# Kernel optimization log

Measured on AMD Instinct MI355X. Metric: run time of the kernel, lower is better.

Reference implementation:

```python
import jax, jax.numpy as jnp
import numpy as np

WINDOW = 128  # window_size from init_kwargs
D = 1024      # input_dim
S = 8192      # seq_len


def setup_inputs() -> dict:
    key = jax.random.key(0)
    k1, k2, k3, k4, k5 = jax.random.split(key, 5)
    bound = 1.0 / np.sqrt(D)
    x = jax.random.normal(k1, (1, S, D), dtype=jnp.float32)
    Wq = jax.random.uniform(k2, (D, D), minval=-bound, maxval=bound, dtype=jnp.float32)
    bq = jax.random.uniform(k3, (D,), minval=-bound, maxval=bound, dtype=jnp.float32)
    Wk = jax.random.uniform(k4, (D, D), minval=-bound, maxval=bound, dtype=jnp.float32)
    bk = jax.random.uniform(k5, (D,), minval=-bound, maxval=bound, dtype=jnp.float32)
    return {"x": x, "Wq": Wq, "bq": bq, "Wk": Wk, "bk": bk}


def reference(x, Wq, bq, Wk, bk):
    # x: [1, S, D]  (original code only works with batch==1)
    xs = x[0]                          # [S, D]
    q = xs @ Wq.T + bq                 # [S, D]
    k = xs @ Wk.T + bk                 # [S, D]
    scores = q @ k.T                   # [S, S] dense, matches original buffer
    t = jnp.arange(S)[:, None]
    s = jnp.arange(S)[None, :]
    # original writes scores only for s in [t-WINDOW, t+WINDOW); elsewhere stays 0
    inwin = (s >= t - WINDOW) & (s < t + WINDOW)
    scores = jnp.where(inwin, scores, 0.0)
    attn = jax.nn.softmax(scores, axis=1)  # softmax INCLUDES the zero entries, as in original
    out = attn @ xs                    # [S, D]
    return out
```

## Files before the change

kernel.cpp:

```cpp
#include <hip/hip_runtime.h>

#define S 8192
#define D 1024
#define WINDOW 128
#define TQ 16
#define UMAX 288
#define BK 32
#define PAD 68
#define BAND 320

typedef __attribute__((ext_vector_type(8))) short short8;
typedef __attribute__((ext_vector_type(4))) float floatx4;
typedef __attribute__((ext_vector_type(4))) unsigned short ushort4v;
typedef unsigned short u16t;

__device__ __forceinline__ float wave_sum(float v) {
  #pragma unroll
  for (int off = 32; off > 0; off >>= 1) v += __shfl_xor(v, off, 64);
  return v;
}
__device__ __forceinline__ float wave_max(float v) {
  #pragma unroll
  for (int off = 32; off > 0; off >>= 1) v = fmaxf(v, __shfl_xor(v, off, 64));
  return v;
}
__device__ __forceinline__ unsigned int f2bf_rn(float f) {
  unsigned int u = __float_as_uint(f);
  return (u + 0x7fffu + ((u >> 16) & 1u)) >> 16;
}

#define GLDS(gp, lp) __builtin_amdgcn_global_load_lds( \
    (const __attribute__((address_space(1))) void*)(gp), \
    (__attribute__((address_space(3))) void*)(lp), 16, 0, 0)


__global__ __launch_bounds__(256) void wuv_kernel(
    const float* __restrict__ Wq, const float* __restrict__ Wk,
    const float* __restrict__ bq, const float* __restrict__ bk,
    float* __restrict__ uu, float* __restrict__ vv, float* __restrict__ cbuf,
    u16t* __restrict__ wqth, u16t* __restrict__ wqtl,
    u16t* __restrict__ wkth, u16t* __restrict__ wktl,
    float* __restrict__ zreg)
{
  __shared__ float tile[64][65];
  __shared__ float cr[4];
  const int t = threadIdx.x;
  if (blockIdx.z == 2) {
    if (blockIdx.y == 0) {
      if (blockIdx.x < 8) {
        const int i  = (blockIdx.x & 3) * 256 + t;
        const int nh = blockIdx.x >> 2;
        float us = 0.f, vs = 0.f;
        for (int n = nh * 512; n < nh * 512 + 512; ++n) {
          us += Wq[(size_t)n * D + i] * bk[n];
          vs += Wk[(size_t)n * D + i] * bq[n];
        }
        uu[(size_t)nh * D + i] = us;
        vv[(size_t)nh * D + i] = vs;
      } else if (blockIdx.x == 8) {
        float cs = 0.f;
        for (int n = t; n < D; n += 256) cs += bq[n] * bk[n];
        cs = wave_sum(cs);
        if ((t & 63) == 0) cr[t >> 6] = cs;
        __syncthreads();
        if (t == 0) cbuf[0] = cr[0] + cr[1] + cr[2] + cr[3];
      }
    } else {
      int fb  = (blockIdx.y - 1) * 16 + blockIdx.x;
      int idx = fb * 256 + t;
      if (idx < D + 2 * S) zreg[idx] = 0.f;
    }
    return;
  }
  const float* W = blockIdx.z ? Wk : Wq;
  u16t* oh = blockIdx.z ? wkth : wqth;
  u16t* ol = blockIdx.z ? wktl : wqtl;
  const int n0 = blockIdx.x * 64;
  const int i0 = blockIdx.y * 64;
  #pragma unroll
  for (int p = 0; p < 4; ++p) {
    int r = (t >> 4) + p * 16;
    int c = (t & 15) * 4;
    float4 vf = *(const float4*)(W + (size_t)(n0 + r) * D + i0 + c);
    tile[r][c+0] = vf.x; tile[r][c+1] = vf.y; tile[r][c+2] = vf.z; tile[r][c+3] = vf.w;
  }
  __syncthreads();
  #pragma unroll
  for (int p = 0; p < 4; ++p) {
    int ii = (t >> 4) + p * 16;
    int nn = (t & 15) * 4;
    ushort4v h, l;
    #pragma unroll
    for (int e = 0; e < 4; ++e) {
      float f = tile[nn + e][ii];
      unsigned int hb = f2bf_rn(f);
      float hf = __uint_as_float(hb << 16);
      h[e] = (u16t)hb;
      l[e] = (u16t)f2bf_rn(f - hf);
    }
    size_t idx = (size_t)(i0 + ii) * D + n0 + nn;
    *(ushort4v*)(oh + idx) = h;
    *(ushort4v*)(ol + idx) = l;
  }
}

__global__ __launch_bounds__(256) void prep_kernel(
    const float* __restrict__ x, const float* __restrict__ uu,
    const float* __restrict__ vv, u16t* __restrict__ xhi, u16t* __restrict__ xlo,
    u16t* __restrict__ xT, float* __restrict__ xsum,
    float* __restrict__ a, float* __restrict__ b)
{
  __shared__ float tile[64][65];
  const int s0 = blockIdx.x * 64;
  const int d0 = blockIdx.y * 64;
  const int t = threadIdx.x;
  #pragma unroll
  for (int p = 0; p < 4; ++p) {
    int r = (t >> 4) + p * 16;
    int c = (t & 15) * 4;
    float4 vf = *(const float4*)(x + (size_t)(s0 + r) * D + d0 + c);
    float f[4] = {vf.x, vf.y, vf.z, vf.w};
    tile[r][c+0] = vf.x; tile[r][c+1] = vf.y; tile[r][c+2] = vf.z; tile[r][c+3] = vf.w;
    ushort4v h, l;
    #pragma unroll
    for (int e = 0; e < 4; ++e) {
      unsigned int hb = f2bf_rn(f[e]);
      float hf = __uint_as_float(hb << 16);
      h[e] = (u16t)hb;
      l[e] = (u16t)f2bf_rn(f[e] - hf);
    }
    size_t idx = (size_t)(s0 + r) * D + d0 + c;
    *(ushort4v*)(xhi + idx) = h;
    *(ushort4v*)(xlo + idx) = l;
  }
  __syncthreads();
  #pragma unroll
  for (int p = 0; p < 4; ++p) {
    int dd = (t >> 4) + p * 16;
    int ss = (t & 15) * 4;
    ushort4v o;
    #pragma unroll
    for (int e = 0; e < 4; ++e) o[e] = (u16t)f2bf_rn(tile[ss + e][dd]);
    *(ushort4v*)(xT + (size_t)(d0 + dd) * S + s0 + ss) = o;
  }
  if (t < 64) {
    float s = 0.f;
    #pragma unroll 8
    for (int r = 0; r < 64; ++r) s += tile[r][t];
    atomicAdd(&xsum[d0 + t], s);
  } else if (t < 128) {
    int r = t - 64;
    float s = 0.f;
    for (int c = 0; c < 64; ++c) s += tile[r][c] * (uu[d0 + c] + uu[D + d0 + c]);
    atomicAdd(&a[s0 + r], s);
  } else if (t < 192) {
    int r = t - 128;
    float s = 0.f;
    for (int c = 0; c < 64; ++c) s += tile[r][c] * (vv[d0 + c] + vv[D + d0 + c]);
    atomicAdd(&b[s0 + r], s);
  }
}

__global__ __launch_bounds__(256) void m_kernel(
    const u16t* __restrict__ wqth, const u16t* __restrict__ wqtl,
    const u16t* __restrict__ wkth, const u16t* __restrict__ wktl,
    u16t* __restrict__ mh, u16t* __restrict__ ml)
{
  __shared__ __align__(16) u16t Mbuf[4][64 * BK];

  const int tid  = threadIdx.x;
  const int lane = tid & 63;
  const int wv   = tid >> 6;
  const int i0   = blockIdx.x * 64;
  const int j0   = blockIdx.y * 64;

  floatx4 acc[2][2] = {};
  const int m0w = (wv & 1) * 32;
  const int n0w = (wv >> 1) * 32;
  const int srow = lane >> 2;
  const int scolw = ((lane & 3) ^ ((lane >> 3) & 3)) * 8;
  const int rs    = (((lane >> 4) ^ ((lane >> 1) & 3)) * 8);

  for (int k0 = 0; k0 < D; k0 += BK) {
    __syncthreads();
    {
      const u16t* src = (wv == 0) ? wqth : (wv == 1) ? wqtl : (wv == 2) ? wkth : wktl;
      const int base  = (wv < 2) ? i0 : j0;
      #pragma unroll
      for (int sg = 0; sg < 4; ++sg) {
        int row = base + sg * 16 + srow;
        size_t g = (size_t)row * D + k0 + scolw;
        GLDS(src + g, &Mbuf[wv][sg * 512]);
      }
    }
    __syncthreads();
    short8 ah[2], al[2], bh[2], bl[2];
    #pragma unroll
    for (int t = 0; t < 2; ++t) {
      int ar = (m0w + t * 16 + (lane & 15)) * BK + rs;
      int br = (n0w + t * 16 + (lane & 15)) * BK + rs;
      ah[t] = *(const short8*)&Mbuf[0][ar];
      al[t] = *(const short8*)&Mbuf[1][ar];
      bh[t] = *(const short8*)&Mbuf[2][br];
      bl[t] = *(const short8*)&Mbuf[3][br];
    }
    #pragma unroll
    for (int mt = 0; mt < 2; ++mt)
      #pragma unroll
      for (int nt = 0; nt < 2; ++nt) {
        acc[mt][nt] = __builtin_amdgcn_mfma_f32_16x16x32_bf16(ah[mt], bh[nt], acc[mt][nt], 0, 0, 0);
        acc[mt][nt] = __builtin_amdgcn_mfma_f32_16x16x32_bf16(ah[mt], bl[nt], acc[mt][nt], 0, 0, 0);
        acc[mt][nt] = __builtin_amdgcn_mfma_f32_16x16x32_bf16(al[mt], bh[nt], acc[mt][nt], 0, 0, 0);
      }
  }
  #pragma unroll
  for (int mt = 0; mt < 2; ++mt)
    #pragma unroll
    for (int nt = 0; nt < 2; ++nt) {
      int j = j0 + n0w + nt * 16 + (lane & 15);
      int i = i0 + m0w + mt * 16 + (lane >> 4) * 4;
      #pragma unroll
      for (int r = 0; r < 4; ++r) {
        float f = acc[mt][nt][r];
        unsigned int hb = f2bf_rn(f);
        float hf = __uint_as_float(hb << 16);
        size_t idx = (size_t)(i + r) * D + j;
        mh[idx] = (u16t)hb;
        ml[idx] = (u16t)f2bf_rn(f - hf);
      }
    }
}

__global__ __launch_bounds__(256) void y_kernel(
    const u16t* __restrict__ xhi, const u16t* __restrict__ xlo,
    const u16t* __restrict__ mhp, const u16t* __restrict__ mlp,
    u16t* __restrict__ yh, u16t* __restrict__ yl)
{
  __shared__ __align__(16) u16t Ah[2 * 128 * BK];
  __shared__ __align__(16) u16t Al[2 * 128 * BK];
  __shared__ __align__(16) u16t Bh[2 * 128 * BK];
  __shared__ __align__(16) u16t Bl[2 * 128 * BK];

  const int tid  = threadIdx.x;
  const int lane = tid & 63;
  const int wv   = tid >> 6;
  const int s0   = blockIdx.x * 128;
  const int i0   = blockIdx.y * 128;

  floatx4 acc[4][4] = {};
  const int m0w  = (wv & 1) * 64;
  const int n0w  = (wv >> 1) * 64;
  const int srow = lane >> 2;
  const int scolw = ((lane & 3) ^ ((lane >> 3) & 3)) * 8;
  const int rs    = (((lane >> 4) ^ ((lane >> 1) & 3)) * 8);

  for (int k0 = 0; k0 < D; k0 += 64) {
    __syncthreads();
    #pragma unroll
    for (int h = 0; h < 2; ++h) {
      #pragma unroll
      for (int sg = 0; sg < 2; ++sg) {
        int seg  = wv * 2 + sg;
        int arow = s0 + seg * 16 + srow;
        int brow = i0 + seg * 16 + srow;
        size_t ga = (size_t)arow * D + k0 + h * 32 + scolw;
        size_t gb = (size_t)brow * D + k0 + h * 32 + scolw;
        int lb = h * 4096 + seg * 512;
        GLDS(xhi + ga, &Ah[lb]);
        GLDS(xlo + ga, &Al[lb]);
        GLDS(mhp + gb, &Bh[lb]);
        GLDS(mlp + gb, &Bl[lb]);
      }
    }
    __syncthreads();
    #pragma unroll
    for (int h = 0; h < 2; ++h) {
      short8 ah[4], al[4], bh[4], bl[4];
      #pragma unroll
      for (int t = 0; t < 4; ++t) {
        int ar = h * 4096 + (m0w + t * 16 + (lane & 15)) * BK + rs;
        int br = h * 4096 + (n0w + t * 16 + (lane & 15)) * BK + rs;
        ah[t] = *(const short8*)&Ah[ar];
        al[t] = *(const short8*)&Al[ar];
        bh[t] = *(const short8*)&Bh[br];
        bl[t] = *(const short8*)&Bl[br];
      }
      #pragma unroll
      for (int mt = 0; mt < 4; ++mt)
        #pragma unroll
        for (int nt = 0; nt < 4; ++nt) {
          acc[mt][nt] = __builtin_amdgcn_mfma_f32_16x16x32_bf16(ah[mt], bh[nt], acc[mt][nt], 0, 0, 0);
          acc[mt][nt] = __builtin_amdgcn_mfma_f32_16x16x32_bf16(ah[mt], bl[nt], acc[mt][nt], 0, 0, 0);
          acc[mt][nt] = __builtin_amdgcn_mfma_f32_16x16x32_bf16(al[mt], bh[nt], acc[mt][nt], 0, 0, 0);
        }
    }
  }
  #pragma unroll
  for (int mt = 0; mt < 4; ++mt)
    #pragma unroll
    for (int nt = 0; nt < 4; ++nt) {
      int i = i0 + n0w + nt * 16 + (lane & 15);
      int s = s0 + m0w + mt * 16 + (lane >> 4) * 4;
      #pragma unroll
      for (int r = 0; r < 4; ++r) {
        float f = acc[mt][nt][r];
        unsigned int hb = f2bf_rn(f);
        float hf = __uint_as_float(hb << 16);
        size_t idx = (size_t)(s + r) * D + i;
        yh[idx] = (u16t)hb;
        yl[idx] = (u16t)f2bf_rn(f - hf);
      }
    }
}

__global__ __launch_bounds__(256) void scores_kernel(
    const u16t* __restrict__ xhi, const u16t* __restrict__ xlo,
    const u16t* __restrict__ yh, const u16t* __restrict__ yl,
    const float* __restrict__ a, const float* __restrict__ b,
    const float* __restrict__ cbuf, float* __restrict__ band)
{
  __shared__ __align__(16) u16t Ah[2 * 64 * BK];
  __shared__ __align__(16) u16t Al[2 * 64 * BK];
  __shared__ __align__(16) u16t Bh[2 * 64 * BK];
  __shared__ __align__(16) u16t Bl[2 * 64 * BK];

  const int tid  = threadIdx.x;
  const int lane = tid & 63;
  const int wv   = tid >> 6;
  const int t0   = blockIdx.x * 64;
  const int jt   = blockIdx.y;
  const int s_base = t0 - 128 + jt * 64;
  const float cval = cbuf[0];

  floatx4 acc[2][2] = {};
  const int m0w  = (wv & 1) * 32;
  const int n0w  = (wv >> 1) * 32;
  const int srow = lane >> 2;
  const int scolw = ((lane & 3) ^ ((lane >> 3) & 3)) * 8;
  const int rs    = (((lane >> 4) ^ ((lane >> 1) & 3)) * 8);

  for (int k0 = 0; k0 < D; k0 += 64) {
    __syncthreads();
    #pragma unroll
    for (int h = 0; h < 2; ++h) {
      int arow = t0 + wv * 16 + srow;
      int brow = s_base + wv * 16 + srow;
      brow = min(max(brow, 0), S - 1);
      size_t ga = (size_t)arow * D + k0 + h * 32 + scolw;
      size_t gb = (size_t)brow * D + k0 + h * 32 + scolw;
      int lb = h * 2048 + wv * 512;
      GLDS(xhi + ga, &Ah[lb]);
      GLDS(xlo + ga, &Al[lb]);
      GLDS(yh + gb, &Bh[lb]);
      GLDS(yl + gb, &Bl[lb]);
    }
    __syncthreads();
    #pragma unroll
    for (int h = 0; h < 2; ++h) {
      short8 ah[2], al[2], bh[2], bl[2];
      #pragma unroll
      for (int t = 0; t < 2; ++t) {
        int ar = h * 2048 + (m0w + t * 16 + (lane & 15)) * BK + rs;
        int br = h * 2048 + (n0w + t * 16 + (lane & 15)) * BK + rs;
        ah[t] = *(const short8*)&Ah[ar];
        al[t] = *(const short8*)&Al[ar];
        bh[t] = *(const short8*)&Bh[br];
        bl[t] = *(const short8*)&Bl[br];
      }
      #pragma unroll
      for (int mt = 0; mt < 2; ++mt)
        #pragma unroll
        for (int nt = 0; nt < 2; ++nt) {
          acc[mt][nt] = __builtin_amdgcn_mfma_f32_16x16x32_bf16(ah[mt], bh[nt], acc[mt][nt], 0, 0, 0);
          acc[mt][nt] = __builtin_amdgcn_mfma_f32_16x16x32_bf16(ah[mt], bl[nt], acc[mt][nt], 0, 0, 0);
          acc[mt][nt] = __builtin_amdgcn_mfma_f32_16x16x32_bf16(al[mt], bh[nt], acc[mt][nt], 0, 0, 0);
        }
    }
  }
  #pragma unroll
  for (int mt = 0; mt < 2; ++mt)
    #pragma unroll
    for (int nt = 0; nt < 2; ++nt) {
      int n_loc = n0w + nt * 16 + (lane & 15);
      int s = s_base + n_loc;
      float bv = (s >= 0 && s < S) ? b[s] : 0.f;
      #pragma unroll
      for (int r = 0; r < 4; ++r) {
        int m_loc = m0w + mt * 16 + (lane >> 4) * 4 + r;
        int t = t0 + m_loc;
        bool inwin = (s >= t - WINDOW) && (s < t + WINDOW) && (s >= 0) && (s < S);
        float sv = inwin ? (acc[mt][nt][r] + a[t] + bv + cval) : 0.f;
        band[(size_t)t * BAND + jt * 64 + n_loc] = sv;
      }
    }
}

#define PSTR 328
__global__ __launch_bounds__(256) void pv_kernel(
    const float* __restrict__ band, const u16t* __restrict__ xT,
    const float* __restrict__ xsum, float* __restrict__ out)
{
  __shared__ __align__(16) u16t Pl[64 * PSTR];
  __shared__ __align__(16) u16t Bb[2 * 128 * BK];
  __shared__ float e0s[64];

  const int tid  = threadIdx.x;
  const int lane = tid & 63;
  const int wv   = tid >> 6;
  const int t0   = blockIdx.x * 64;
  const int d0   = blockIdx.y * 128;
  const int origin = t0 - 128;

  for (int it = 0; it < 16; ++it) {
    int rloc = it * 4 + wv;
    const float* row = band + (size_t)(t0 + rloc) * BAND;
    float v[5];
    float mx = 0.f;
    #pragma unroll
    for (int i = 0; i < 5; ++i) {
      v[i] = row[i * 64 + lane];
      mx = fmaxf(mx, v[i]);
    }
    mx = wave_max(mx);
    float e0 = __expf(-mx);
    float ss = 0.f;
    #pragma unroll
    for (int i = 0; i < 5; ++i) {
      v[i] = __expf(v[i] - mx);
      ss += v[i];
    }
    ss = wave_sum(ss);
    float dinv = 1.f / (ss + (float)(S - BAND) * e0);
    #pragma unroll
    for (int i = 0; i < 5; ++i)
      Pl[rloc * PSTR + i * 64 + lane] = (u16t)f2bf_rn((v[i] - e0) * dinv);
    if (lane == 0) e0s[rloc] = e0 * dinv;
  }

  floatx4 acc[2][4] = {};
  const int m0w  = (wv & 1) * 32;
  const int n0w  = (wv >> 1) * 64;
  const int srow = lane >> 2;
  const int scolw = ((lane & 3) ^ ((lane >> 3) & 3)) * 8;
  const int rs    = (((lane >> 4) ^ ((lane >> 1) & 3)) * 8);
  const int fr    = lane & 15;
  const int qA    = (lane >> 4) * 8;

  for (int k0 = 0; k0 < BAND; k0 += 64) {
    __syncthreads();
    #pragma unroll
    for (int h = 0; h < 2; ++h) {
      #pragma unroll
      for (int sg = 0; sg < 2; ++sg) {
        int seg  = wv * 2 + sg;
        int brow = d0 + seg * 16 + srow;
        int s_g  = origin + k0 + h * 32 + scolw;
        s_g = min(max(s_g, 0), S - 8);
        size_t gb = (size_t)brow * S + s_g;
        GLDS(xT + gb, &Bb[h * 4096 + seg * 512]);
      }
    }
    __syncthreads();
    #pragma unroll
    for (int h = 0; h < 2; ++h) {
      short8 af[2], bf[4];
      #pragma unroll
      for (int t = 0; t < 2; ++t)
        af[t] = *(const short8*)&Pl[(m0w + t * 16 + fr) * PSTR + k0 + h * 32 + qA];
      #pragma unroll
      for (int t = 0; t < 4; ++t)
        bf[t] = *(const short8*)&Bb[h * 4096 + (n0w + t * 16 + fr) * BK + rs];
      #pragma unroll
      for (int mt = 0; mt < 2; ++mt)
        #pragma unroll
        for (int nt = 0; nt < 4; ++nt)
          acc[mt][nt] = __builtin_amdgcn_mfma_f32_16x16x32_bf16(af[mt], bf[nt], acc[mt][nt], 0, 0, 0);
    }
  }
  #pragma unroll
  for (int mt = 0; mt < 2; ++mt)
    #pragma unroll
    for (int nt = 0; nt < 4; ++nt) {
      int n_g = d0 + n0w + nt * 16 + fr;
      float xs = xsum[n_g];
      #pragma unroll
      for (int r = 0; r < 4; ++r) {
        int rloc = m0w + mt * 16 + (lane >> 4) * 4 + r;
        out[(size_t)(t0 + rloc) * D + n_g] = acc[mt][nt][r] + e0s[rloc] * xs;
      }
    }
}

__global__ __launch_bounds__(256) void proj_kernel(
    const float* __restrict__ x, const float* __restrict__ Wq,
    const float* __restrict__ bqv, const float* __restrict__ Wk,
    const float* __restrict__ bkv, float* __restrict__ qout,
    float* __restrict__ kout)
{
  __shared__ __align__(16) float xs[BK][PAD];
  __shared__ __align__(16) float wqs[BK][PAD];
  __shared__ __align__(16) float wks[BK][PAD];
  const int tid = threadIdx.x;
  const int tx = tid & 15, ty = tid >> 4;
  const int t0 = blockIdx.x * 64, i0 = blockIdx.y * 64;
  float accq[4][4] = {}, acck[4][4] = {};
  const int lrow0 = tid >> 3, lc4 = (tid & 7) * 4;
  for (int k0 = 0; k0 < D; k0 += BK) {
    __syncthreads();
    #pragma unroll
    for (int p = 0; p < 2; ++p) {
      int row = lrow0 + p * 32;
      float4 a = *(const float4*)(x  + (size_t)(t0 + row) * D + k0 + lc4);
      float4 b = *(const float4*)(Wq + (size_t)(i0 + row) * D + k0 + lc4);
      float4 c = *(const float4*)(Wk + (size_t)(i0 + row) * D + k0 + lc4);
      xs [lc4+0][row]=a.x; xs [lc4+1][row]=a.y; xs [lc4+2][row]=a.z; xs [lc4+3][row]=a.w;
      wqs[lc4+0][row]=b.x; wqs[lc4+1][row]=b.y; wqs[lc4+2][row]=b.z; wqs[lc4+3][row]=b.w;
      wks[lc4+0][row]=c.x; wks[lc4+1][row]=c.y; wks[lc4+2][row]=c.z; wks[lc4+3][row]=c.w;
    }
    __syncthreads();
    #pragma unroll
    for (int kk = 0; kk < BK; ++kk) {
      float4 av = *(const float4*)&xs [kk][ty*4];
      float4 bv = *(const float4*)&wqs[kk][tx*4];
      float4 cv = *(const float4*)&wks[kk][tx*4];
      float a[4] = {av.x, av.y, av.z, av.w};
      float b[4] = {bv.x, bv.y, bv.z, bv.w};
      float c[4] = {cv.x, cv.y, cv.z, cv.w};
      #pragma unroll
      for (int r = 0; r < 4; ++r)
        #pragma unroll
        for (int cc = 0; cc < 4; ++cc) {
          accq[r][cc] = fmaf(a[r], b[cc], accq[r][cc]);
          acck[r][cc] = fmaf(a[r], c[cc], acck[r][cc]);
        }
    }
  }
  float4 bq4 = *(const float4*)(bqv + i0 + tx*4);
  float4 bk4 = *(const float4*)(bkv + i0 + tx*4);
  #pragma unroll
  for (int r = 0; r < 4; ++r) {
    int trow = t0 + ty*4 + r;
    float4 oq = { accq[r][0]+bq4.x, accq[r][1]+bq4.y, accq[r][2]+bq4.z, accq[r][3]+bq4.w };
    float4 ok = { acck[r][0]+bk4.x, acck[r][1]+bk4.y, acck[r][2]+bk4.z, acck[r][3]+bk4.w };
    *(float4*)(qout + (size_t)trow * D + i0 + tx*4) = oq;
    *(float4*)(kout + (size_t)trow * D + i0 + tx*4) = ok;
  }
}

__global__ __launch_bounds__(256) void colsum_kernel(const float* __restrict__ x,
                                                     float* __restrict__ xsum)
{
  int d = blockIdx.x * 256 + threadIdx.x;
  int tbase = blockIdx.y * 256;
  float s = 0.f;
  for (int t = 0; t < 256; ++t) s += x[(size_t)(tbase + t) * D + d];
  atomicAdd(&xsum[d], s);
}

__global__ __launch_bounds__(256) void attn_kernel(
    const float* __restrict__ x, const float* __restrict__ q,
    const float* __restrict__ kmat, const float* __restrict__ xsum,
    float* __restrict__ out)
{
  __shared__ __align__(16) float scl[TQ][UMAX];
  __shared__ float e0s[TQ], dinv[TQ];
  const int tid = threadIdx.x, lane = tid & 63, wv = tid >> 6;
  const int t0 = blockIdx.x * TQ;
  const int lo_u = max(0, t0 - WINDOW);
  const int hi_u = min(S, t0 + TQ - 1 + WINDOW);
  const int ucnt = hi_u - lo_u;
  for (int i = tid; i < TQ * UMAX; i += 256) (&scl[0][0])[i] = 0.f;
  __syncthreads();
  {
    const int tiB = wv * 4;
    float4 qf[4][4];
    #pragma unroll
    for (int g = 0; g < 4; ++g) {
      int t = t0 + tiB + g;
      #pragma unroll
      for (int j = 0; j < 4; ++j)
        qf[g][j] = *(const float4*)(q + (size_t)t * D + lane*4 + j*256);
    }
    const int wlo = max(0, t0 + tiB - WINDOW);
    const int whi = min(S, t0 + tiB + 3 + WINDOW);
    for (int s = wlo; s < whi; ++s) {
      float4 kf[4];
      #pragma unroll
      for (int j = 0; j < 4; ++j)
        kf[j] = *(const float4*)(kmat + (size_t)s * D + lane*4 + j*256);
      float acc[4];
      #pragma unroll
      for (int g = 0; g < 4; ++g) {
        float v = 0.f;
        #pragma unroll
        for (int j = 0; j < 4; ++j) {
          v = fmaf(qf[g][j].x, kf[j].x, v);
          v = fmaf(qf[g][j].y, kf[j].y, v);
          v = fmaf(qf[g][j].z, kf[j].z, v);
          v = fmaf(qf[g][j].w, kf[j].w, v);
        }
        acc[g] = v;
      }
      #pragma unroll
      for (int g = 0; g < 4; ++g) {
        float tot = wave_sum(acc[g]);
        int t = t0 + tiB + g;
        if (lane == 0 && s >= t - WINDOW && s < t + WINDOW)
          scl[tiB + g][s - lo_u] = tot;
      }
    }
  }
  __syncthreads();
  #pragma unroll
  for (int g = 0; g < 4; ++g) {
    int ti = wv * 4 + g;
    int t = t0 + ti;
    int lo = max(0, t - WINDOW), hi = min(S, t + WINDOW);
    int cnt = hi - lo, off = lo - lo_u;
    float m = 0.f;
    for (int i = lane; i < cnt; i += 64) m = fmaxf(m, scl[ti][off + i]);
    m = wave_max(m);
    float e0 = __expf(-m);
    float ssum = 0.f;
    for (int i = lane; i < cnt; i += 64) {
      float e = __expf(scl[ti][off + i] - m);
      ssum += e;
      scl[ti][off + i] = e - e0;
    }
    ssum = wave_sum(ssum);
    if (lane == 0) {
      dinv[ti] = 1.f / (ssum + (float)(S - cnt) * e0);
      e0s[ti] = e0;
    }
  }
  __syncthreads();
  {
    const int c4 = tid * 4;
    float4 acc[TQ];
    #pragma unroll
    for (int ti = 0; ti < TQ; ++ti) acc[ti] = make_float4(0.f, 0.f, 0.f, 0.f);
    for (int su = 0; su < ucnt; su += 4) {
      float4 xr[4];
      #pragma unroll
      for (int u = 0; u < 4; ++u)
        xr[u] = *(const float4*)(x + (size_t)(lo_u + su + u) * D + c4);
      #pragma unroll
      for (int ti = 0; ti < TQ; ++ti) {
        float4 w4 = *(const float4*)&scl[ti][su];
        float wvv[4] = {w4.x, w4.y, w4.z, w4.w};
        #pragma unroll
        for (int u = 0; u < 4; ++u) {
          acc[ti].x = fmaf(wvv[u], xr[u].x, acc[ti].x);
          acc[ti].y = fmaf(wvv[u], xr[u].y, acc[ti].y);
          acc[ti].z = fmaf(wvv[u], xr[u].z, acc[ti].z);
          acc[ti].w = fmaf(wvv[u], xr[u].w, acc[ti].w);
        }
      }
    }
    float4 xsv = *(const float4*)(xsum + c4);
    #pragma unroll
    for (int ti = 0; ti < TQ; ++ti) {
      float e0 = e0s[ti], di = dinv[ti];
      float4 o;
      o.x = (acc[ti].x + e0 * xsv.x) * di;
      o.y = (acc[ti].y + e0 * xsv.y) * di;
      o.z = (acc[ti].z + e0 * xsv.z) * di;
      o.w = (acc[ti].w + e0 * xsv.w) * di;
      *(float4*)(out + (size_t)(t0 + ti) * D + c4) = o;
    }
  }
}

extern "C" void kernel_launch(void* const* d_in, const int* in_sizes, int n_in,
                              void* d_out, int out_size, void* d_ws, size_t ws_size,
                              hipStream_t stream) {
  const float* x  = (const float*)d_in[0];
  const float* Wq = (const float*)d_in[1];
  const float* bq = (const float*)d_in[2];
  const float* Wk = (const float*)d_in[3];
  const float* bk = (const float*)d_in[4];
  float* outp = (float*)d_out;

  const size_t SD = (size_t)S * D;
  const size_t DD = (size_t)D * D;

  float* xsum = (float*)d_ws;
  float* a    = xsum + D;
  float* b    = a + S;
  float* uu   = b + S;
  float* vv   = uu + 2 * D;
  float* cbuf = vv + 2 * D;

  u16t* xhi  = (u16t*)(cbuf + 16);
  u16t* xlo  = xhi + SD;
  u16t* xT   = xlo + SD;
  u16t* wqth = xT + SD;
  u16t* wqtl = wqth + DD;
  u16t* wkth = wqtl + DD;
  u16t* wktl = wkth + DD;
  u16t* mh   = wktl + DD;
  u16t* ml   = mh + DD;
  u16t* yh   = ml + DD;
  u16t* yl   = yh + SD;
  float* band = (float*)(yl + SD);
  size_t needed = (size_t)((char*)(band + (size_t)S * BAND) - (char*)d_ws);

  if (ws_size >= needed) {
    wuv_kernel<<<dim3(16, 16, 3), 256, 0, stream>>>(
        Wq, Wk, bq, bk, uu, vv, cbuf, wqth, wqtl, wkth, wktl, xsum);
    prep_kernel<<<dim3(S / 64, D / 64), 256, 0, stream>>>(x, uu, vv, xhi, xlo, xT, xsum, a, b);
    m_kernel<<<dim3(D / 64, D / 64), 256, 0, stream>>>(wqth, wqtl, wkth, wktl, mh, ml);
    y_kernel<<<dim3(S / 128, D / 128), 256, 0, stream>>>(xhi, xlo, mh, ml, yh, yl);
    scores_kernel<<<dim3(S / 64, 5), 256, 0, stream>>>(xhi, xlo, yh, yl, a, b, cbuf, band);
    pv_kernel<<<dim3(S / 64, D / 128), 256, 0, stream>>>(band, xT, xsum, outp);
  } else {
    float* xs2  = (float*)d_ws;
    float* q    = xs2 + D;
    float* kbuf = q + SD;
    (void)hipMemsetAsync(xs2, 0, D * sizeof(float), stream);
    colsum_kernel<<<dim3(D / 256, S / 256), 256, 0, stream>>>(x, xs2);
    proj_kernel<<<dim3(S / 64, D / 64), 256, 0, stream>>>(x, Wq, bq, Wk, bk, q, kbuf);
    attn_kernel<<<S / TQ, 256, 0, stream>>>(x, q, kbuf, xs2, outp);
  }
}
```

Measured before the change: 293.2 us.

## Switch GEMMs to 32x32x16 MFMA and split softmax out of PV kernel

```diff
diff --git a/kernel.cpp b/kernel.cpp
--- a/kernel.cpp
+++ b/kernel.cpp
@@ -11,6 +11,7 @@
 
 typedef __attribute__((ext_vector_type(8))) short short8;
 typedef __attribute__((ext_vector_type(4))) float floatx4;
+typedef __attribute__((ext_vector_type(16))) float floatx16;
 typedef __attribute__((ext_vector_type(4))) unsigned short ushort4v;
 typedef unsigned short u16t;
 
@@ -174,12 +175,14 @@
   const int i0   = blockIdx.x * 64;
   const int j0   = blockIdx.y * 64;
 
-  floatx4 acc[2][2] = {};
+  floatx16 acc = {};
   const int m0w = (wv & 1) * 32;
   const int n0w = (wv >> 1) * 32;
   const int srow = lane >> 2;
   const int scolw = ((lane & 3) ^ ((lane >> 3) & 3)) * 8;
-  const int rs    = (((lane >> 4) ^ ((lane >> 1) & 3)) * 8);
+  const int rsw = (lane >> 1) & 3;
+  const int l31 = lane & 31;
+  const int khi = lane >> 5;
 
   for (int k0 = 0; k0 < D; k0 += BK) {
     __syncthreads();
@@ -194,41 +197,34 @@
       }
     }
     __syncthreads();
-    short8 ah[2], al[2], bh[2], bl[2];
-    #pragma unroll
-    for (int t = 0; t < 2; ++t) {
-      int ar = (m0w + t * 16 + (lane & 15)) * BK + rs;
-      int br = (n0w + t * 16 + (lane & 15)) * BK + rs;
-      ah[t] = *(const short8*)&Mbuf[0][ar];
-      al[t] = *(const short8*)&Mbuf[1][ar];
-      bh[t] = *(const short8*)&Mbuf[2][br];
-      bl[t] = *(const short8*)&Mbuf[3][br];
-    }
-    #pragma unroll
-    for (int mt = 0; mt < 2; ++mt)
-      #pragma unroll
-      for (int nt = 0; nt < 2; ++nt) {
-        acc[mt][nt] = __builtin_amdgcn_mfma_f32_16x16x32_bf16(ah[mt], bh[nt], acc[mt][nt], 0, 0, 0);
-        acc[mt][nt] = __builtin_amdgcn_mfma_f32_16x16x32_bf16(ah[mt], bl[nt], acc[mt][nt], 0, 0, 0);
-        acc[mt][nt] = __builtin_amdgcn_mfma_f32_16x16x32_bf16(al[mt], bh[nt], acc[mt][nt], 0, 0, 0);
-      }
-  }
-  #pragma unroll
-  for (int mt = 0; mt < 2; ++mt)
-    #pragma unroll
-    for (int nt = 0; nt < 2; ++nt) {
-      int j = j0 + n0w + nt * 16 + (lane & 15);
-      int i = i0 + m0w + mt * 16 + (lane >> 4) * 4;
-      #pragma unroll
-      for (int r = 0; r < 4; ++r) {
-        float f = acc[mt][nt][r];
-        unsigned int hb = f2bf_rn(f);
-        float hf = __uint_as_float(hb << 16);
-        size_t idx = (size_t)(i + r) * D + j;
-        mh[idx] = (u16t)hb;
-        ml[idx] = (u16t)f2bf_rn(f - hf);
-      }
-    }
+    #pragma unroll
+    for (int ks = 0; ks < 2; ++ks) {
+      int slot = ((ks * 2 + khi) ^ rsw) * 8;
+      int ar = (m0w + l31) * BK + slot;
+      int br = (n0w + l31) * BK + slot;
+      short8 ah = *(const short8*)&Mbuf[0][ar];
+      short8 al = *(const short8*)&Mbuf[1][ar];
+      short8 bh = *(const short8*)&Mbuf[2][br];
+      short8 bl = *(const short8*)&Mbuf[3][br];
+      acc = __builtin_amdgcn_mfma_f32_32x32x16_bf16(ah, bh, acc, 0, 0, 0);
+      acc = __builtin_amdgcn_mfma_f32_32x32x16_bf16(ah, bl, acc, 0, 0, 0);
+      acc = __builtin_amdgcn_mfma_f32_32x32x16_bf16(al, bh, acc, 0, 0, 0);
+    }
+  }
+  {
+    int j = j0 + n0w + l31;
+    int ib = i0 + m0w + 4 * khi;
+    #pragma unroll
+    for (int r = 0; r < 16; ++r) {
+      int i = ib + (r & 3) + 8 * (r >> 2);
+      float f = acc[r];
+      unsigned int hb = f2bf_rn(f);
+      float hf = __uint_as_float(hb << 16);
+      size_t idx = (size_t)i * D + j;
+      mh[idx] = (u16t)hb;
+      ml[idx] = (u16t)f2bf_rn(f - hf);
+    }
+  }
 }
 
 __global__ __launch_bounds__(256) void y_kernel(
@@ -247,12 +243,14 @@
   const int s0   = blockIdx.x * 128;
   const int i0   = blockIdx.y * 128;
 
-  floatx4 acc[4][4] = {};
+  floatx16 acc[2][2] = {};
   const int m0w  = (wv & 1) * 64;
   const int n0w  = (wv >> 1) * 64;
   const int srow = lane >> 2;
   const int scolw = ((lane & 3) ^ ((lane >> 3) & 3)) * 8;
-  const int rs    = (((lane >> 4) ^ ((lane >> 1) & 3)) * 8);
+  const int rsw = (lane >> 1) & 3;
+  const int l31 = lane & 31;
+  const int khi = lane >> 5;
 
   for (int k0 = 0; k0 < D; k0 += 64) {
     __syncthreads();
@@ -275,38 +273,43 @@
     __syncthreads();
     #pragma unroll
     for (int h = 0; h < 2; ++h) {
-      short8 ah[4], al[4], bh[4], bl[4];
-      #pragma unroll
-      for (int t = 0; t < 4; ++t) {
-        int ar = h * 4096 + (m0w + t * 16 + (lane & 15)) * BK + rs;
-        int br = h * 4096 + (n0w + t * 16 + (lane & 15)) * BK + rs;
-        ah[t] = *(const short8*)&Ah[ar];
-        al[t] = *(const short8*)&Al[ar];
-        bh[t] = *(const short8*)&Bh[br];
-        bl[t] = *(const short8*)&Bl[br];
-      }
-      #pragma unroll
-      for (int mt = 0; mt < 4; ++mt)
+      #pragma unroll
+      for (int ks = 0; ks < 2; ++ks) {
+        int slot = ((ks * 2 + khi) ^ rsw) * 8;
+        short8 ah[2], al[2], bh[2], bl[2];
         #pragma unroll
-        for (int nt = 0; nt < 4; ++nt) {
-          acc[mt][nt] = __builtin_amdgcn_mfma_f32_16x16x32_bf16(ah[mt], bh[nt], acc[mt][nt], 0, 0, 0);
-          acc[mt][nt] = __builtin_amdgcn_mfma_f32_16x16x32_bf16(ah[mt], bl[nt], acc[mt][nt], 0, 0, 0);
-          acc[mt][nt] = __builtin_amdgcn_mfma_f32_16x16x32_bf16(al[mt], bh[nt], acc[mt][nt], 0, 0, 0);
+        for (int t = 0; t < 2; ++t) {
+          int ar = h * 4096 + (m0w + t * 32 + l31) * BK + slot;
+          int br = h * 4096 + (n0w + t * 32 + l31) * BK + slot;
+          ah[t] = *(const short8*)&Ah[ar];
+          al[t] = *(const short8*)&Al[ar];
+          bh[t] = *(const short8*)&Bh[br];
+          bl[t] = *(const short8*)&Bl[br];
         }
-    }
-  }
-  #pragma unroll
-  for (int mt = 0; mt < 4; ++mt)
-    #pragma unroll
-    for (int nt = 0; nt < 4; ++nt) {
-      int i = i0 + n0w + nt * 16 + (lane & 15);
-      int s = s0 + m0w + mt * 16 + (lane >> 4) * 4;
-      #pragma unroll
-      for (int r = 0; r < 4; ++r) {
+        #pragma unroll
+        for (int mt = 0; mt < 2; ++mt)
+          #pragma unroll
+          for (int nt = 0; nt < 2; ++nt) {
+            acc[mt][nt] = __builtin_amdgcn_mfma_f32_32x32x16_bf16(ah[mt], bh[nt], acc[mt][nt], 0, 0, 0);
+            acc[mt][nt] = __builtin_amdgcn_mfma_f32_32x32x16_bf16(ah[mt], bl[nt], acc[mt][nt], 0, 0, 0);
+            acc[mt][nt] = __builtin_amdgcn_mfma_f32_32x32x16_bf16(al[mt], bh[nt], acc[mt][nt], 0, 0, 0);
+          }
+      }
+    }
+  }
+  #pragma unroll
+  for (int mt = 0; mt < 2; ++mt)
+    #pragma unroll
+    for (int nt = 0; nt < 2; ++nt) {
+      int i  = i0 + n0w + nt * 32 + l31;
+      int sb = s0 + m0w + mt * 32 + 4 * khi;
+      #pragma unroll
+      for (int r = 0; r < 16; ++r) {
+        int s = sb + (r & 3) + 8 * (r >> 2);
         float f = acc[mt][nt][r];
         unsigned int hb = f2bf_rn(f);
         float hf = __uint_as_float(hb << 16);
-        size_t idx = (size_t)(s + r) * D + i;
+        size_t idx = (size_t)s * D + i;
         yh[idx] = (u16t)hb;
         yl[idx] = (u16t)f2bf_rn(f - hf);
       }
@@ -332,12 +335,14 @@
   const int s_base = t0 - 128 + jt * 64;
   const float cval = cbuf[0];
 
-  floatx4 acc[2][2] = {};
+  floatx16 acc = {};
   const int m0w  = (wv & 1) * 32;
   const int n0w  = (wv >> 1) * 32;
   const int srow = lane >> 2;
   const int scolw = ((lane & 3) ^ ((lane >> 3) & 3)) * 8;
-  const int rs    = (((lane >> 4) ^ ((lane >> 1) & 3)) * 8);
+  const int rsw = (lane >> 1) & 3;
+  const int l31 = lane & 31;
+  const int khi = lane >> 5;
 
   for (int k0 = 0; k0 < D; k0 += 64) {
     __syncthreads();
@@ -357,52 +362,74 @@
     __syncthreads();
     #pragma unroll
     for (int h = 0; h < 2; ++h) {
-      short8 ah[2], al[2], bh[2], bl[2];
-      #pragma unroll
-      for (int t = 0; t < 2; ++t) {
-        int ar = h * 2048 + (m0w + t * 16 + (lane & 15)) * BK + rs;
-        int br = h * 2048 + (n0w + t * 16 + (lane & 15)) * BK + rs;
-        ah[t] = *(const short8*)&Ah[ar];
-        al[t] = *(const short8*)&Al[ar];
-        bh[t] = *(const short8*)&Bh[br];
-        bl[t] = *(const short8*)&Bl[br];
-      }
-      #pragma unroll
-      for (int mt = 0; mt < 2; ++mt)
-        #pragma unroll
-        for (int nt = 0; nt < 2; ++nt) {
-          acc[mt][nt] = __builtin_amdgcn_mfma_f32_16x16x32_bf16(ah[mt], bh[nt], acc[mt][nt], 0, 0, 0);
-          acc[mt][nt] = __builtin_amdgcn_mfma_f32_16x16x32_bf16(ah[mt], bl[nt], acc[mt][nt], 0, 0, 0);
-          acc[mt][nt] = __builtin_amdgcn_mfma_f32_16x16x32_bf16(al[mt], bh[nt], acc[mt][nt], 0, 0, 0);
-        }
-    }
-  }
-  #pragma unroll
-  for (int mt = 0; mt < 2; ++mt)
-    #pragma unroll
-    for (int nt = 0; nt < 2; ++nt) {
-      int n_loc = n0w + nt * 16 + (lane & 15);
-      int s = s_base + n_loc;
-      float bv = (s >= 0 && s < S) ? b[s] : 0.f;
-      #pragma unroll
-      for (int r = 0; r < 4; ++r) {
-        int m_loc = m0w + mt * 16 + (lane >> 4) * 4 + r;
-        int t = t0 + m_loc;
-        bool inwin = (s >= t - WINDOW) && (s < t + WINDOW) && (s >= 0) && (s < S);
-        float sv = inwin ? (acc[mt][nt][r] + a[t] + bv + cval) : 0.f;
-        band[(size_t)t * BAND + jt * 64 + n_loc] = sv;
-      }
-    }
-}
-
-#define PSTR 328
+      #pragma unroll
+      for (int ks = 0; ks < 2; ++ks) {
+        int slot = ((ks * 2 + khi) ^ rsw) * 8;
+        int ar = h * 2048 + (m0w + l31) * BK + slot;
+        int br = h * 2048 + (n0w + l31) * BK + slot;
+        short8 ah = *(const short8*)&Ah[ar];
+        short8 al = *(const short8*)&Al[ar];
+        short8 bh = *(const short8*)&Bh[br];
+        short8 bl = *(const short8*)&Bl[br];
+        acc = __builtin_amdgcn_mfma_f32_32x32x16_bf16(ah, bh, acc, 0, 0, 0);
+        acc = __builtin_amdgcn_mfma_f32_32x32x16_bf16(ah, bl, acc, 0, 0, 0);
+        acc = __builtin_amdgcn_mfma_f32_32x32x16_bf16(al, bh, acc, 0, 0, 0);
+      }
+    }
+  }
+  {
+    int n_loc = n0w + l31;
+    int s = s_base + n_loc;
+    float bv = (s >= 0 && s < S) ? b[s] : 0.f;
+    int mb = m0w + 4 * khi;
+    #pragma unroll
+    for (int r = 0; r < 16; ++r) {
+      int m_loc = mb + (r & 3) + 8 * (r >> 2);
+      int t = t0 + m_loc;
+      bool inwin = (s >= t - WINDOW) && (s < t + WINDOW) && (s >= 0) && (s < S);
+      float sv = inwin ? (acc[r] + a[t] + bv + cval) : 0.f;
+      band[(size_t)t * BAND + jt * 64 + n_loc] = sv;
+    }
+  }
+}
+
+__global__ __launch_bounds__(256) void softmax_kernel(
+    const float* __restrict__ band, u16t* __restrict__ Pb, float* __restrict__ e0d)
+{
+  const int lane = threadIdx.x & 63;
+  const int w    = threadIdx.x >> 6;
+  const int t    = blockIdx.x * 4 + w;
+  const float* row = band + (size_t)t * BAND;
+  float v[5];
+  float mx = 0.f;
+  #pragma unroll
+  for (int i = 0; i < 5; ++i) {
+    v[i] = row[i * 64 + lane];
+    mx = fmaxf(mx, v[i]);
+  }
+  mx = wave_max(mx);
+  float e0 = __expf(-mx);
+  float ss = 0.f;
+  #pragma unroll
+  for (int i = 0; i < 5; ++i) {
+    v[i] = __expf(v[i] - mx);
+    ss += v[i];
+  }
+  ss = wave_sum(ss);
+  float dinv = 1.f / (ss + (float)(S - BAND) * e0);
+  #pragma unroll
+  for (int i = 0; i < 5; ++i)
+    Pb[(size_t)t * BAND + i * 64 + lane] = (u16t)f2bf_rn((v[i] - e0) * dinv);
+  if (lane == 0) e0d[t] = e0 * dinv;
+}
+
 __global__ __launch_bounds__(256) void pv_kernel(
-    const float* __restrict__ band, const u16t* __restrict__ xT,
-    const float* __restrict__ xsum, float* __restrict__ out)
-{
-  __shared__ __align__(16) u16t Pl[64 * PSTR];
+    const u16t* __restrict__ Pb, const u16t* __restrict__ xT,
+    const float* __restrict__ e0d, const float* __restrict__ xsum,
+    float* __restrict__ out)
+{
+  __shared__ __align__(16) u16t Ab[2 * 64 * BK];
   __shared__ __align__(16) u16t Bb[2 * 128 * BK];
-  __shared__ float e0s[64];
 
   const int tid  = threadIdx.x;
   const int lane = tid & 63;
@@ -411,45 +438,25 @@
   const int d0   = blockIdx.y * 128;
   const int origin = t0 - 128;
 
-  for (int it = 0; it < 16; ++it) {
-    int rloc = it * 4 + wv;
-    const float* row = band + (size_t)(t0 + rloc) * BAND;
-    float v[5];
-    float mx = 0.f;
-    #pragma unroll
-    for (int i = 0; i < 5; ++i) {
-      v[i] = row[i * 64 + lane];
-      mx = fmaxf(mx, v[i]);
-    }
-    mx = wave_max(mx);
-    float e0 = __expf(-mx);
-    float ss = 0.f;
-    #pragma unroll
-    for (int i = 0; i < 5; ++i) {
-      v[i] = __expf(v[i] - mx);
-      ss += v[i];
-    }
-    ss = wave_sum(ss);
-    float dinv = 1.f / (ss + (float)(S - BAND) * e0);
-    #pragma unroll
-    for (int i = 0; i < 5; ++i)
-      Pl[rloc * PSTR + i * 64 + lane] = (u16t)f2bf_rn((v[i] - e0) * dinv);
-    if (lane == 0) e0s[rloc] = e0 * dinv;
-  }
-
-  floatx4 acc[2][4] = {};
+  floatx16 acc[2] = {};
   const int m0w  = (wv & 1) * 32;
   const int n0w  = (wv >> 1) * 64;
   const int srow = lane >> 2;
   const int scolw = ((lane & 3) ^ ((lane >> 3) & 3)) * 8;
-  const int rs    = (((lane >> 4) ^ ((lane >> 1) & 3)) * 8);
-  const int fr    = lane & 15;
-  const int qA    = (lane >> 4) * 8;
+  const int rsw = (lane >> 1) & 3;
+  const int l31 = lane & 31;
+  const int khi = lane >> 5;
 
   for (int k0 = 0; k0 < BAND; k0 += 64) {
     __syncthreads();
     #pragma unroll
     for (int h = 0; h < 2; ++h) {
+      {
+        int arow = t0 + wv * 16 + srow;
+        size_t ga = (size_t)arow * BAND + k0 + h * 32 + scolw;
+        int lb = h * 2048 + wv * 512;
+        GLDS(Pb + ga, &Ab[lb]);
+      }
       #pragma unroll
       for (int sg = 0; sg < 2; ++sg) {
         int seg  = wv * 2 + sg;
@@ -457,38 +464,38 @@
         int s_g  = origin + k0 + h * 32 + scolw;
         s_g = min(max(s_g, 0), S - 8);
         size_t gb = (size_t)brow * S + s_g;
-        GLDS(xT + gb, &Bb[h * 4096 + seg * 512]);
+        int lb = h * 4096 + seg * 512;
+        GLDS(xT + gb, &Bb[lb]);
       }
     }
     __syncthreads();
     #pragma unroll
     for (int h = 0; h < 2; ++h) {
-      short8 af[2], bf[4];
-      #pragma unroll
-      for (int t = 0; t < 2; ++t)
-        af[t] = *(const short8*)&Pl[(m0w + t * 16 + fr) * PSTR + k0 + h * 32 + qA];
-      #pragma unroll
-      for (int t = 0; t < 4; ++t)
-        bf[t] = *(const short8*)&Bb[h * 4096 + (n0w + t * 16 + fr) * BK + rs];
-      #pragma unroll
-      for (int mt = 0; mt < 2; ++mt)
+      #pragma unroll
+      for (int ks = 0; ks < 2; ++ks) {
+        int slot = ((ks * 2 + khi) ^ rsw) * 8;
+        short8 af = *(const short8*)&Ab[h * 2048 + (m0w + l31) * BK + slot];
+        short8 bf[2];
         #pragma unroll
-        for (int nt = 0; nt < 4; ++nt)
-          acc[mt][nt] = __builtin_amdgcn_mfma_f32_16x16x32_bf16(af[mt], bf[nt], acc[mt][nt], 0, 0, 0);
-    }
-  }
-  #pragma unroll
-  for (int mt = 0; mt < 2; ++mt)
-    #pragma unroll
-    for (int nt = 0; nt < 4; ++nt) {
-      int n_g = d0 + n0w + nt * 16 + fr;
-      float xs = xsum[n_g];
-      #pragma unroll
-      for (int r = 0; r < 4; ++r) {
-        int rloc = m0w + mt * 16 + (lane >> 4) * 4 + r;
-        out[(size_t)(t0 + rloc) * D + n_g] = acc[mt][nt][r] + e0s[rloc] * xs;
-      }
-    }
+        for (int t = 0; t < 2; ++t)
+          bf[t] = *(const short8*)&Bb[h * 4096 + (n0w + t * 32 + l31) * BK + slot];
+        #pragma unroll
+        for (int nt = 0; nt < 2; ++nt)
+          acc[nt] = __builtin_amdgcn_mfma_f32_32x32x16_bf16(af, bf[nt], acc[nt], 0, 0, 0);
+      }
+    }
+  }
+  #pragma unroll
+  for (int nt = 0; nt < 2; ++nt) {
+    int n_g = d0 + n0w + nt * 32 + l31;
+    float xs = xsum[n_g];
+    int mb = t0 + m0w + 4 * khi;
+    #pragma unroll
+    for (int r = 0; r < 16; ++r) {
+      int m_g = mb + (r & 3) + 8 * (r >> 2);
+      out[(size_t)m_g * D + n_g] = acc[nt][r] + e0d[m_g] * xs;
+    }
+  }
 }
 
 __global__ __launch_bounds__(256) void proj_kernel(
@@ -703,7 +710,9 @@
   u16t* yh   = ml + DD;
   u16t* yl   = yh + SD;
   float* band = (float*)(yl + SD);
-  size_t needed = (size_t)((char*)(band + (size_t)S * BAND) - (char*)d_ws);
+  u16t*  Pb   = (u16t*)(band + (size_t)S * BAND);
+  float* e0d  = (float*)(Pb + (size_t)S * BAND);
+  size_t needed = (size_t)((char*)(e0d + S) - (char*)d_ws);
 
   if (ws_size >= needed) {
     wuv_kernel<<<dim3(16, 16, 3), 256, 0, stream>>>(
@@ -712,7 +721,8 @@
     m_kernel<<<dim3(D / 64, D / 64), 256, 0, stream>>>(wqth, wqtl, wkth, wktl, mh, ml);
     y_kernel<<<dim3(S / 128, D / 128), 256, 0, stream>>>(xhi, xlo, mh, ml, yh, yl);
     scores_kernel<<<dim3(S / 64, 5), 256, 0, stream>>>(xhi, xlo, yh, yl, a, b, cbuf, band);
-    pv_kernel<<<dim3(S / 64, D / 128), 256, 0, stream>>>(band, xT, xsum, outp);
+    softmax_kernel<<<S / 4, 256, 0, stream>>>(band, Pb, e0d);
+    pv_kernel<<<dim3(S / 64, D / 128), 256, 0, stream>>>(Pb, xT, e0d, xsum, outp);
   } else {
     float* xs2  = (float*)d_ws;
     float* q    = xs2 + D;
```

Result: no change. 289.7 us (-1.2%).

## Split softmax into its own kernel and swizzle y_kernel block order

Applied to the files above, without the earlier changes.

```diff
diff --git a/kernel.cpp b/kernel.cpp
--- a/kernel.cpp
+++ b/kernel.cpp
@@ -244,8 +244,10 @@
   const int tid  = threadIdx.x;
   const int lane = tid & 63;
   const int wv   = tid >> 6;
-  const int s0   = blockIdx.x * 128;
-  const int i0   = blockIdx.y * 128;
+  const int bid  = blockIdx.y * gridDim.x + blockIdx.x;
+  const int sw   = (bid & 7) * 64 + (bid >> 3);
+  const int s0   = (sw & 63) * 128;
+  const int i0   = (sw >> 6) * 128;
 
   floatx4 acc[4][4] = {};
   const int m0w  = (wv & 1) * 64;
@@ -395,14 +397,43 @@
     }
 }
 
-#define PSTR 328
+__global__ __launch_bounds__(256) void softmax_kernel(
+    const float* __restrict__ band, u16t* __restrict__ Pb, float* __restrict__ e0d)
+{
+  const int lane = threadIdx.x & 63;
+  const int w    = threadIdx.x >> 6;
+  const int t    = blockIdx.x * 4 + w;
+  const float* row = band + (size_t)t * BAND;
+  float v[5];
+  float mx = 0.f;
+  #pragma unroll
+  for (int i = 0; i < 5; ++i) {
+    v[i] = row[i * 64 + lane];
+    mx = fmaxf(mx, v[i]);
+  }
+  mx = wave_max(mx);
+  float e0 = __expf(-mx);
+  float ss = 0.f;
+  #pragma unroll
+  for (int i = 0; i < 5; ++i) {
+    v[i] = __expf(v[i] - mx);
+    ss += v[i];
+  }
+  ss = wave_sum(ss);
+  float dinv = 1.f / (ss + (float)(S - BAND) * e0);
+  #pragma unroll
+  for (int i = 0; i < 5; ++i)
+    Pb[(size_t)t * BAND + i * 64 + lane] = (u16t)f2bf_rn((v[i] - e0) * dinv);
+  if (lane == 0) e0d[t] = e0 * dinv;
+}
+
 __global__ __launch_bounds__(256) void pv_kernel(
-    const float* __restrict__ band, const u16t* __restrict__ xT,
-    const float* __restrict__ xsum, float* __restrict__ out)
-{
-  __shared__ __align__(16) u16t Pl[64 * PSTR];
+    const u16t* __restrict__ Pb, const u16t* __restrict__ xT,
+    const float* __restrict__ e0d, const float* __restrict__ xsum,
+    float* __restrict__ out)
+{
+  __shared__ __align__(16) u16t Ab[2 * 64 * BK];
   __shared__ __align__(16) u16t Bb[2 * 128 * BK];
-  __shared__ float e0s[64];
 
   const int tid  = threadIdx.x;
   const int lane = tid & 63;
@@ -411,45 +442,23 @@
   const int d0   = blockIdx.y * 128;
   const int origin = t0 - 128;
 
-  for (int it = 0; it < 16; ++it) {
-    int rloc = it * 4 + wv;
-    const float* row = band + (size_t)(t0 + rloc) * BAND;
-    float v[5];
-    float mx = 0.f;
-    #pragma unroll
-    for (int i = 0; i < 5; ++i) {
-      v[i] = row[i * 64 + lane];
-      mx = fmaxf(mx, v[i]);
-    }
-    mx = wave_max(mx);
-    float e0 = __expf(-mx);
-    float ss = 0.f;
-    #pragma unroll
-    for (int i = 0; i < 5; ++i) {
-      v[i] = __expf(v[i] - mx);
-      ss += v[i];
-    }
-    ss = wave_sum(ss);
-    float dinv = 1.f / (ss + (float)(S - BAND) * e0);
-    #pragma unroll
-    for (int i = 0; i < 5; ++i)
-      Pl[rloc * PSTR + i * 64 + lane] = (u16t)f2bf_rn((v[i] - e0) * dinv);
-    if (lane == 0) e0s[rloc] = e0 * dinv;
-  }
-
   floatx4 acc[2][4] = {};
   const int m0w  = (wv & 1) * 32;
   const int n0w  = (wv >> 1) * 64;
   const int srow = lane >> 2;
   const int scolw = ((lane & 3) ^ ((lane >> 3) & 3)) * 8;
   const int rs    = (((lane >> 4) ^ ((lane >> 1) & 3)) * 8);
-  const int fr    = lane & 15;
-  const int qA    = (lane >> 4) * 8;
 
   for (int k0 = 0; k0 < BAND; k0 += 64) {
     __syncthreads();
     #pragma unroll
     for (int h = 0; h < 2; ++h) {
+      {
+        int arow = t0 + wv * 16 + srow;
+        size_t ga = (size_t)arow * BAND + k0 + h * 32 + scolw;
+        int lb = h * 2048 + wv * 512;
+        GLDS(Pb + ga, &Ab[lb]);
+      }
       #pragma unroll
       for (int sg = 0; sg < 2; ++sg) {
         int seg  = wv * 2 + sg;
@@ -457,7 +466,8 @@
         int s_g  = origin + k0 + h * 32 + scolw;
         s_g = min(max(s_g, 0), S - 8);
         size_t gb = (size_t)brow * S + s_g;
-        GLDS(xT + gb, &Bb[h * 4096 + seg * 512]);
+        int lb = h * 4096 + seg * 512;
+        GLDS(xT + gb, &Bb[lb]);
       }
     }
     __syncthreads();
@@ -465,11 +475,15 @@
     for (int h = 0; h < 2; ++h) {
       short8 af[2], bf[4];
       #pragma unroll
-      for (int t = 0; t < 2; ++t)
-        af[t] = *(const short8*)&Pl[(m0w + t * 16 + fr) * PSTR + k0 + h * 32 + qA];
-      #pragma unroll
-      for (int t = 0; t < 4; ++t)
-        bf[t] = *(const short8*)&Bb[h * 4096 + (n0w + t * 16 + fr) * BK + rs];
+      for (int t = 0; t < 2; ++t) {
+        int ar = h * 2048 + (m0w + t * 16 + (lane & 15)) * BK + rs;
+        af[t] = *(const short8*)&Ab[ar];
+      }
+      #pragma unroll
+      for (int t = 0; t < 4; ++t) {
+        int br = h * 4096 + (n0w + t * 16 + (lane & 15)) * BK + rs;
+        bf[t] = *(const short8*)&Bb[br];
+      }
       #pragma unroll
       for (int mt = 0; mt < 2; ++mt)
         #pragma unroll
@@ -481,12 +495,12 @@
   for (int mt = 0; mt < 2; ++mt)
     #pragma unroll
     for (int nt = 0; nt < 4; ++nt) {
-      int n_g = d0 + n0w + nt * 16 + fr;
+      int n_g = d0 + n0w + nt * 16 + (lane & 15);
       float xs = xsum[n_g];
       #pragma unroll
       for (int r = 0; r < 4; ++r) {
-        int rloc = m0w + mt * 16 + (lane >> 4) * 4 + r;
-        out[(size_t)(t0 + rloc) * D + n_g] = acc[mt][nt][r] + e0s[rloc] * xs;
+        int m_g = t0 + m0w + mt * 16 + (lane >> 4) * 4 + r;
+        out[(size_t)m_g * D + n_g] = acc[mt][nt][r] + e0d[m_g] * xs;
       }
     }
 }
@@ -703,7 +717,9 @@
   u16t* yh   = ml + DD;
   u16t* yl   = yh + SD;
   float* band = (float*)(yl + SD);
-  size_t needed = (size_t)((char*)(band + (size_t)S * BAND) - (char*)d_ws);
+  u16t*  Pb   = (u16t*)(band + (size_t)S * BAND);
+  float* e0d  = (float*)(Pb + (size_t)S * BAND);
+  size_t needed = (size_t)((char*)(e0d + S) - (char*)d_ws);
 
   if (ws_size >= needed) {
     wuv_kernel<<<dim3(16, 16, 3), 256, 0, stream>>>(
@@ -712,7 +728,8 @@
     m_kernel<<<dim3(D / 64, D / 64), 256, 0, stream>>>(wqth, wqtl, wkth, wktl, mh, ml);
     y_kernel<<<dim3(S / 128, D / 128), 256, 0, stream>>>(xhi, xlo, mh, ml, yh, yl);
     scores_kernel<<<dim3(S / 64, 5), 256, 0, stream>>>(xhi, xlo, yh, yl, a, b, cbuf, band);
-    pv_kernel<<<dim3(S / 64, D / 128), 256, 0, stream>>>(band, xT, xsum, outp);
+    softmax_kernel<<<S / 4, 256, 0, stream>>>(band, Pb, e0d);
+    pv_kernel<<<dim3(S / 64, D / 128), 256, 0, stream>>>(Pb, xT, e0d, xsum, outp);
   } else {
     float* xs2  = (float*)d_ws;
     float* q    = xs2 + D;
```

New measurement: 288.0 us. No clear change (-1.8%).
